# Performance work log

Measured on AMD Instinct MI355X. Metric: run time of the kernel, lower is better.

Reference implementation:

```python
import jax, jax.numpy as jnp
import numpy as np

N_HEAD = 16
NEG_BIG = 1e10  # matches the torch module's -10000000000.0 additive mask


def setup_inputs() -> dict:
    key = jax.random.key(0)
    k1, k2, k3 = jax.random.split(key, 3)
    B, T, D = 2, 2048, 1024
    x = jax.random.normal(k1, (B, T, D), dtype=jnp.float32)
    W_attn = jax.random.normal(k2, (D, 3 * D), dtype=jnp.float32) * 0.02
    b_attn = jnp.zeros((3 * D,), dtype=jnp.float32)
    W_proj = jax.random.normal(k3, (D, D), dtype=jnp.float32) * 0.02
    b_proj = jnp.zeros((D,), dtype=jnp.float32)
    return {"x": x, "W_attn": W_attn, "b_attn": b_attn,
            "W_proj": W_proj, "b_proj": b_proj}


def reference(x, W_attn, b_attn, W_proj, b_proj):
    B, T, D = x.shape
    H = N_HEAD
    dh = D // H
    # c_attn: fused qkv projection
    qkv = x @ W_attn + b_attn                      # [B, T, 3D]
    q, k, v = jnp.split(qkv, 3, axis=-1)
    # split heads -> [B, H, T, dh]
    q = q.reshape(B, T, H, dh).transpose(0, 2, 1, 3)
    k = k.reshape(B, T, H, dh).transpose(0, 2, 1, 3)
    v = v.reshape(B, T, H, dh).transpose(0, 2, 1, 3)
    # scores [B, H, T, T]
    w = jnp.einsum("bhqd,bhkd->bhqk", q, k)
    w = w / jnp.sqrt(jnp.float32(dh))              # scale=True
    # causal additive mask: w*b - 1e10*(1-b), b = lower-triangular ones
    bias = jnp.tril(jnp.ones((T, T), dtype=w.dtype))
    w = w * bias - NEG_BIG * (1.0 - bias)
    w = jax.nn.softmax(w, axis=-1)
    a = jnp.einsum("bhqk,bhkd->bhqd", w, v)        # [B, H, T, dh]
    # merge heads
    a = a.transpose(0, 2, 1, 3).reshape(B, T, D)
    # c_proj
    return a @ W_proj + b_proj
```

## Files before the change

### kernel.cpp

```cpp
#include <hip/hip_runtime.h>
#include <hip/hip_bf16.h>


typedef unsigned short u16;
typedef unsigned int u32;
typedef __attribute__((ext_vector_type(4))) float f32x4;
typedef __attribute__((ext_vector_type(16))) float f32x16;
typedef __attribute__((ext_vector_type(8))) short bf16x8;
typedef __attribute__((ext_vector_type(4))) int i32x4;

__device__ __forceinline__ u16 f2bf(float f) {
  unsigned u = __builtin_bit_cast(unsigned, f);
  u += 0x7FFFu + ((u >> 16) & 1u);
  return (u16)(u >> 16);
}

__device__ __forceinline__ u32 pack_bf2(float lo, float hi) {
  return (u32)f2bf(lo) | ((u32)f2bf(hi) << 16);
}

__device__ __forceinline__ void gl_lds16(const u16* g, u16* l) {
  __builtin_amdgcn_global_load_lds(
      (const __attribute__((address_space(1))) void*)g,
      (__attribute__((address_space(3))) void*)l, 16, 0, 0);
}

__global__ __launch_bounds__(256) void cast_bf16_kernel(const float* __restrict__ in,
                                                        u16* __restrict__ out, int n4) {
  int i = blockIdx.x * 256 + threadIdx.x;
  if (i < n4) {
    float4 f = reinterpret_cast<const float4*>(in)[i];
    ushort4 o;
    o.x = f2bf(f.x); o.y = f2bf(f.y); o.z = f2bf(f.z); o.w = f2bf(f.w);
    reinterpret_cast<ushort4*>(out)[i] = o;
  }
}

__global__ __launch_bounds__(256) void transpose_cast(const float* __restrict__ in,
                                                      u16* __restrict__ out, int R, int C) {
  __shared__ float tile[32][33];
  const int c0 = blockIdx.x * 32, r0 = blockIdx.y * 32;
  const int tx = threadIdx.x, ty = threadIdx.y;
#pragma unroll
  for (int i = 0; i < 4; ++i)
    tile[ty + 8 * i][tx] = in[(size_t)(r0 + ty + 8 * i) * C + c0 + tx];
  __syncthreads();
#pragma unroll
  for (int i = 0; i < 4; ++i)
    out[(size_t)(c0 + ty + 8 * i) * R + r0 + tx] = f2bf(tile[tx][ty + 8 * i]);
}

template <int MODE>
__global__ __launch_bounds__(256) void gemm_bf16(
    const u16* __restrict__ A, const u16* __restrict__ Bt, const float* __restrict__ bias,
    float* __restrict__ outF, u16* __restrict__ Qh, u16* __restrict__ Kh, u16* __restrict__ VhT,
    int M, int N, int K) {
  __shared__ u16 As[128 * 32];
  __shared__ u16 Bs[128 * 32];
  const int tid = threadIdx.x;
  const int wave = tid >> 6, lane = tid & 63;
  const int kg = lane >> 4, rr = lane & 15;
  const int wm = wave >> 1, wn = wave & 1;
  const int rowA0 = blockIdx.y * 128, colB0 = blockIdx.x * 128;

  const f32x4 z4 = {0.f, 0.f, 0.f, 0.f};
  f32x4 acc[4][4];
#pragma unroll
  for (int i = 0; i < 4; ++i)
#pragma unroll
    for (int j = 0; j < 4; ++j) acc[i][j] = z4;

  const int r_st = tid >> 2;
  const int c_st = (tid & 3) * 8;

  for (int k0 = 0; k0 < K; k0 += 32) {
#pragma unroll
    for (int i = 0; i < 2; ++i) {
      gl_lds16(A + (size_t)(rowA0 + i * 64 + r_st) * K + k0 + c_st,
               As + (i * 256 + (wave << 6)) * 8);
      gl_lds16(Bt + (size_t)(colB0 + i * 64 + r_st) * K + k0 + c_st,
               Bs + (i * 256 + (wave << 6)) * 8);
    }
    __syncthreads();

    bf16x8 af[4], bfr[4];
#pragma unroll
    for (int mi = 0; mi < 4; ++mi)
      af[mi] = *reinterpret_cast<const bf16x8*>(&As[(wm * 64 + mi * 16 + rr) * 32 + kg * 8]);
#pragma unroll
    for (int ni = 0; ni < 4; ++ni)
      bfr[ni] = *reinterpret_cast<const bf16x8*>(&Bs[(wn * 64 + ni * 16 + rr) * 32 + kg * 8]);
#pragma unroll
    for (int mi = 0; mi < 4; ++mi)
#pragma unroll
      for (int ni = 0; ni < 4; ++ni)
        acc[mi][ni] = __builtin_amdgcn_mfma_f32_16x16x32_bf16(af[mi], bfr[ni], acc[mi][ni], 0, 0, 0);
    __syncthreads();
  }

#pragma unroll
  for (int mi = 0; mi < 4; ++mi) {
#pragma unroll
    for (int ni = 0; ni < 4; ++ni) {
      const int col = colB0 + wn * 64 + ni * 16 + rr;
      const float bcol = bias[col];
      f32x4 a = acc[mi][ni];
#pragma unroll
      for (int v = 0; v < 4; ++v) {
        const int row = rowA0 + wm * 64 + mi * 16 + kg * 4 + v;
        const float val = a[v] + bcol;
        if (MODE == 1) {
          outF[(size_t)row * N + col] = val;
        } else {
          const int b = row >> 11, t = row & 2047;
          const int which = col >> 10, d = col & 1023;
          const int h = d >> 6, dd = d & 63;
          const size_t bh = (size_t)(b * 16 + h);
          if (which == 0)
            Qh[(bh * 2048 + t) * 64 + dd] = f2bf(val);
          else if (which == 1)
            Kh[(bh * 2048 + t) * 64 + dd] = f2bf(val);
          else
            VhT[(bh * 64 + dd) * 2048 + t] = f2bf(val);
        }
      }
    }
  }
}

__global__ __launch_bounds__(256) void attn_fwd(const u16* __restrict__ Qh,
                                                const u16* __restrict__ Kh,
                                                const u16* __restrict__ VhT,
                                                u16* __restrict__ Ab) {
  const int tid = threadIdx.x;
  const int wave = tid >> 6, lane = tid & 63;
  const int lq = lane & 31, hi = lane >> 5;
  const int task = blockIdx.x * 4 + wave;
  const int qi = task >> 5;
  const int bh = task & 31;
  const int qtile = 63 - qi;
  const int q0 = qtile * 32;
  const int myq = q0 + lq;
  const size_t kvbase = (size_t)bh * 2048;

  bf16x8 qf[4];
  {
    const u16* qptr = Qh + (kvbase + q0 + lq) * 64 + hi * 8;
#pragma unroll
    for (int ks = 0; ks < 4; ++ks)
      qf[ks] = *reinterpret_cast<const bf16x8*>(qptr + ks * 16);
  }

  f32x16 oA, oB;
#pragma unroll
  for (int i = 0; i < 16; ++i) { oA[i] = 0.f; oB[i] = 0.f; }
  float m = -1e30f, l = 0.f;

  const int n64 = (q0 + 32 + 63) >> 6;
  for (int kvb = 0; kvb < n64; ++kvb) {
    const int kv0 = kvb * 64;

    const u16* kptr = Kh + (kvbase + kv0 + lq) * 64 + hi * 8;
    bf16x8 kfA[4], kfB[4];
#pragma unroll
    for (int ks = 0; ks < 4; ++ks) {
      kfA[ks] = *reinterpret_cast<const bf16x8*>(kptr + ks * 16);
      kfB[ks] = *reinterpret_cast<const bf16x8*>(kptr + 2048 + ks * 16);
    }
    const u16* vptr = VhT + ((size_t)bh * 64 + lq) * 2048 + kv0 + hi * 8;
    bf16x8 vfA[4], vfB[4];
#pragma unroll
    for (int ks = 0; ks < 4; ++ks) {
      vfA[ks] = *reinterpret_cast<const bf16x8*>(vptr + ks * 16);
      vfB[ks] = *reinterpret_cast<const bf16x8*>(vptr + 32 * 2048 + ks * 16);
    }

    f32x16 sA, sB;
#pragma unroll
    for (int i = 0; i < 16; ++i) { sA[i] = 0.f; sB[i] = 0.f; }
#pragma unroll
    for (int ks = 0; ks < 4; ++ks)
      sA = __builtin_amdgcn_mfma_f32_32x32x16_bf16(kfA[ks], qf[ks], sA, 0, 0, 0);
#pragma unroll
    for (int ks = 0; ks < 4; ++ks)
      sB = __builtin_amdgcn_mfma_f32_32x32x16_bf16(kfB[ks], qf[ks], sB, 0, 0, 0);

    if (kvb == n64 - 1) {
#pragma unroll
      for (int r = 0; r < 16; ++r) {
        const int kvA = kv0 + (r & 3) + 8 * (r >> 2) + 4 * hi;
        if (kvA > myq) sA[r] = -1e30f;
        if (kvA + 32 > myq) sB[r] = -1e30f;
      }
    }

    float pmax = -1e30f;
#pragma unroll
    for (int r = 0; r < 16; ++r) pmax = fmaxf(pmax, fmaxf(sA[r], sB[r]));
    pmax = fmaxf(pmax, __shfl_xor(pmax, 32));
    const float mn = fmaxf(m, pmax);
    const float sc = __expf((m - mn) * 0.125f);
    const float mn8 = mn * 0.125f;
    float rsum = 0.f;
#pragma unroll
    for (int r = 0; r < 16; ++r) {
      const float pa = __expf(__builtin_fmaf(sA[r], 0.125f, -mn8));
      const float pb = __expf(__builtin_fmaf(sB[r], 0.125f, -mn8));
      sA[r] = pa; sB[r] = pb;
      rsum += pa + pb;
    }
    rsum += __shfl_xor(rsum, 32);
    l = l * sc + rsum;
    m = mn;
    oA *= sc;
    oB *= sc;

    u32 pkA[8], pkB[8];
#pragma unroll
    for (int i = 0; i < 8; ++i) {
      pkA[i] = pack_bf2(sA[2 * i], sA[2 * i + 1]);
      pkB[i] = pack_bf2(sB[2 * i], sB[2 * i + 1]);
    }
    bf16x8 pf[4];
    {
      auto w0 = __builtin_amdgcn_permlane32_swap(pkA[0], pkA[2], false, false);
      auto w1 = __builtin_amdgcn_permlane32_swap(pkA[1], pkA[3], false, false);
      i32x4 t0 = {(int)w0[0], (int)w1[0], (int)w0[1], (int)w1[1]};
      pf[0] = __builtin_bit_cast(bf16x8, t0);
      auto w2 = __builtin_amdgcn_permlane32_swap(pkA[4], pkA[6], false, false);
      auto w3 = __builtin_amdgcn_permlane32_swap(pkA[5], pkA[7], false, false);
      i32x4 t1 = {(int)w2[0], (int)w3[0], (int)w2[1], (int)w3[1]};
      pf[1] = __builtin_bit_cast(bf16x8, t1);
      auto w4 = __builtin_amdgcn_permlane32_swap(pkB[0], pkB[2], false, false);
      auto w5 = __builtin_amdgcn_permlane32_swap(pkB[1], pkB[3], false, false);
      i32x4 t2 = {(int)w4[0], (int)w5[0], (int)w4[1], (int)w5[1]};
      pf[2] = __builtin_bit_cast(bf16x8, t2);
      auto w6 = __builtin_amdgcn_permlane32_swap(pkB[4], pkB[6], false, false);
      auto w7 = __builtin_amdgcn_permlane32_swap(pkB[5], pkB[7], false, false);
      i32x4 t3 = {(int)w6[0], (int)w7[0], (int)w6[1], (int)w7[1]};
      pf[3] = __builtin_bit_cast(bf16x8, t3);
    }

#pragma unroll
    for (int ks = 0; ks < 4; ++ks)
      oA = __builtin_amdgcn_mfma_f32_32x32x16_bf16(vfA[ks], pf[ks], oA, 0, 0, 0);
#pragma unroll
    for (int ks = 0; ks < 4; ++ks)
      oB = __builtin_amdgcn_mfma_f32_32x32x16_bf16(vfB[ks], pf[ks], oB, 0, 0, 0);
  }

  const float inv = 1.0f / l;
  const int b = bh >> 4, h = bh & 15;
  u16* base = Ab + ((size_t)b * 2048 + myq) * 1024 + h * 64;
#pragma unroll
  for (int g = 0; g < 4; ++g) {
    const int dh0 = 8 * g + 4 * hi;
    ushort4 wa, wb;
    wa.x = f2bf(oA[4 * g + 0] * inv); wa.y = f2bf(oA[4 * g + 1] * inv);
    wa.z = f2bf(oA[4 * g + 2] * inv); wa.w = f2bf(oA[4 * g + 3] * inv);
    wb.x = f2bf(oB[4 * g + 0] * inv); wb.y = f2bf(oB[4 * g + 1] * inv);
    wb.z = f2bf(oB[4 * g + 2] * inv); wb.w = f2bf(oB[4 * g + 3] * inv);
    *reinterpret_cast<ushort4*>(base + dh0) = wa;
    *reinterpret_cast<ushort4*>(base + 32 + dh0) = wb;
  }
}

extern "C" void kernel_launch(void* const* d_in, const int* in_sizes, int n_in,
                              void* d_out, int out_size, void* d_ws, size_t ws_size,
                              hipStream_t stream) {
  const float* x      = (const float*)d_in[0];
  const float* W_attn = (const float*)d_in[1];
  const float* b_attn = (const float*)d_in[2];
  const float* W_proj = (const float*)d_in[3];
  const float* b_proj = (const float*)d_in[4];
  float* out = (float*)d_out;

  u16* xb  = (u16*)d_ws;
  u16* Wat = xb + (size_t)4096 * 1024;
  u16* Wpt = Wat + (size_t)3072 * 1024;
  u16* Qh  = Wpt + (size_t)1024 * 1024;
  u16* Kh  = Qh + (size_t)4194304;
  u16* VhT = Kh + (size_t)4194304;
  u16* Ab  = VhT + (size_t)4194304;

  cast_bf16_kernel<<<4096, 256, 0, stream>>>(x, xb, 4096 * 1024 / 4);
  transpose_cast<<<dim3(96, 32), dim3(32, 8), 0, stream>>>(W_attn, Wat, 1024, 3072);
  transpose_cast<<<dim3(32, 32), dim3(32, 8), 0, stream>>>(W_proj, Wpt, 1024, 1024);
  gemm_bf16<0><<<dim3(24, 32), 256, 0, stream>>>(xb, Wat, b_attn, nullptr, Qh, Kh, VhT,
                                                 4096, 3072, 1024);
  attn_fwd<<<dim3(512), 256, 0, stream>>>(Qh, Kh, VhT, Ab);
  gemm_bf16<1><<<dim3(8, 32), 256, 0, stream>>>(Ab, Wpt, b_proj, out, nullptr, nullptr, nullptr,
                                                4096, 1024, 1024);
}
```

Baseline: 247.1 us.

## Split attention KV range across waves, swizzle GEMM tiles, lazy softmax rescale

The attention kernel now gives each block one (q-tile, head) pair and splits its KV blocks across four waves. The per-wave partial max, sum and output are merged through LDS before a single store. This raises the block count from 512 to 2048 to improve load balance and occupancy for the causal triangle. The 1/8 softmax scale is folded into Q during the QKV GEMM, and the running-max rescale is skipped when the max grows by no more than 8, which is a lazy rescaling trick. Both GEMMs get an XCD-style block swizzle, and the projection GEMM uses narrower 128x64 tiles for more blocks. In exchange it adds LDS traffic, a sync, and a small bf16 accuracy change from prescaling Q.

Measured after the change: 225.5 us. 8.7% less time.

```diff
diff --git a/kernel.cpp b/kernel.cpp
--- a/kernel.cpp
+++ b/kernel.cpp
@@ -50,18 +50,20 @@
     out[(size_t)(c0 + ty + 8 * i) * R + r0 + tx] = f2bf(tile[tx][ty + 8 * i]);
 }
 
-template <int MODE>
-__global__ __launch_bounds__(256) void gemm_bf16(
+__global__ __launch_bounds__(256) void gemm_qkv(
     const u16* __restrict__ A, const u16* __restrict__ Bt, const float* __restrict__ bias,
-    float* __restrict__ outF, u16* __restrict__ Qh, u16* __restrict__ Kh, u16* __restrict__ VhT,
-    int M, int N, int K) {
+    u16* __restrict__ Qh, u16* __restrict__ Kh, u16* __restrict__ VhT, int K) {
   __shared__ u16 As[128 * 32];
   __shared__ u16 Bs[128 * 32];
   const int tid = threadIdx.x;
   const int wave = tid >> 6, lane = tid & 63;
   const int kg = lane >> 4, rr = lane & 15;
   const int wm = wave >> 1, wn = wave & 1;
-  const int rowA0 = blockIdx.y * 128, colB0 = blockIdx.x * 128;
+  const int nwg = gridDim.x * gridDim.y;
+  const int lin = blockIdx.y * gridDim.x + blockIdx.x;
+  const int swz = (lin & 7) * (nwg >> 3) + (lin >> 3);
+  const int bx = swz % gridDim.x, by = swz / gridDim.x;
+  const int rowA0 = by * 128, colB0 = bx * 128;
 
   const f32x4 z4 = {0.f, 0.f, 0.f, 0.f};
   f32x4 acc[4][4];
@@ -109,20 +111,79 @@
       for (int v = 0; v < 4; ++v) {
         const int row = rowA0 + wm * 64 + mi * 16 + kg * 4 + v;
         const float val = a[v] + bcol;
-        if (MODE == 1) {
-          outF[(size_t)row * N + col] = val;
-        } else {
-          const int b = row >> 11, t = row & 2047;
-          const int which = col >> 10, d = col & 1023;
-          const int h = d >> 6, dd = d & 63;
-          const size_t bh = (size_t)(b * 16 + h);
-          if (which == 0)
-            Qh[(bh * 2048 + t) * 64 + dd] = f2bf(val);
-          else if (which == 1)
-            Kh[(bh * 2048 + t) * 64 + dd] = f2bf(val);
-          else
-            VhT[(bh * 64 + dd) * 2048 + t] = f2bf(val);
-        }
+        const int b = row >> 11, t = row & 2047;
+        const int which = col >> 10, d = col & 1023;
+        const int h = d >> 6, dd = d & 63;
+        const size_t bh = (size_t)(b * 16 + h);
+        if (which == 0)
+          Qh[(bh * 2048 + t) * 64 + dd] = f2bf(val * 0.125f);
+        else if (which == 1)
+          Kh[(bh * 2048 + t) * 64 + dd] = f2bf(val);
+        else
+          VhT[(bh * 64 + dd) * 2048 + t] = f2bf(val);
+      }
+    }
+  }
+}
+
+__global__ __launch_bounds__(256) void gemm_proj(
+    const u16* __restrict__ A, const u16* __restrict__ Bt, const float* __restrict__ bias,
+    float* __restrict__ outF, int N, int K) {
+  __shared__ u16 As[128 * 32];
+  __shared__ u16 Bs[64 * 32];
+  const int tid = threadIdx.x;
+  const int wave = tid >> 6, lane = tid & 63;
+  const int kg = lane >> 4, rr = lane & 15;
+  const int nwg = gridDim.x * gridDim.y;
+  const int lin = blockIdx.y * gridDim.x + blockIdx.x;
+  const int swz = (lin & 7) * (nwg >> 3) + (lin >> 3);
+  const int bx = swz % gridDim.x, by = swz / gridDim.x;
+  const int rowA0 = by * 128, colB0 = bx * 64;
+
+  const f32x4 z4 = {0.f, 0.f, 0.f, 0.f};
+  f32x4 acc[2][4];
+#pragma unroll
+  for (int i = 0; i < 2; ++i)
+#pragma unroll
+    for (int j = 0; j < 4; ++j) acc[i][j] = z4;
+
+  const int r_st = tid >> 2;
+  const int c_st = (tid & 3) * 8;
+
+  for (int k0 = 0; k0 < K; k0 += 32) {
+#pragma unroll
+    for (int i = 0; i < 2; ++i)
+      gl_lds16(A + (size_t)(rowA0 + i * 64 + r_st) * K + k0 + c_st,
+               As + (i * 256 + (wave << 6)) * 8);
+    gl_lds16(Bt + (size_t)(colB0 + r_st) * K + k0 + c_st, Bs + (wave << 6) * 8);
+    __syncthreads();
+
+    bf16x8 af[2], bfr[4];
+#pragma unroll
+    for (int mi = 0; mi < 2; ++mi)
+      af[mi] = *reinterpret_cast<const bf16x8*>(&As[(wave * 32 + mi * 16 + rr) * 32 + kg * 8]);
+#pragma unroll
+    for (int ni = 0; ni < 4; ++ni)
+      bfr[ni] = *reinterpret_cast<const bf16x8*>(&Bs[(ni * 16 + rr) * 32 + kg * 8]);
+#pragma unroll
+    for (int mi = 0; mi < 2; ++mi)
+#pragma unroll
+      for (int ni = 0; ni < 4; ++ni)
+        acc[mi][ni] = __builtin_amdgcn_mfma_f32_16x16x32_bf16(af[mi], bfr[ni], acc[mi][ni], 0, 0, 0);
+    __syncthreads();
+  }
+
+#pragma unroll
+  for (int mi = 0; mi < 2; ++mi) {
+#pragma unroll
+    for (int ni = 0; ni < 4; ++ni) {
+      const int col = colB0 + ni * 16 + rr;
+      const float bcol = bias[col];
+      f32x4 a = acc[mi][ni];
+#pragma unroll
+      for (int v = 0; v < 4; ++v) {
+        const int row = rowA0 + wave * 32 + mi * 16 + kg * 4 + v;
+        outF[(size_t)row * N + col] = a[v] + bcol;
       }
     }
   }
@@ -132,17 +193,24 @@
                                                 const u16* __restrict__ Kh,
                                                 const u16* __restrict__ VhT,
                                                 u16* __restrict__ Ab) {
+  __shared__ float Ol[4][64][33];
+  __shared__ float Ml[4][2][32];
   const int tid = threadIdx.x;
   const int wave = tid >> 6, lane = tid & 63;
   const int lq = lane & 31, hi = lane >> 5;
-  const int task = blockIdx.x * 4 + wave;
-  const int qi = task >> 5;
-  const int bh = task & 31;
+  const int blk = blockIdx.x;
+  const int qi = blk >> 5;
+  const int bh = blk & 31;
   const int qtile = 63 - qi;
   const int q0 = qtile * 32;
   const int myq = q0 + lq;
   const size_t kvbase = (size_t)bh * 2048;
 
+  const int n64 = (q0 + 32 + 63) >> 6;
+  const int base = n64 >> 2, rem = n64 & 3;
+  const int cnt = base + (wave < rem ? 1 : 0);
+  const int start = wave * base + (wave < rem ? wave : rem);
+
   bf16x8 qf[4];
   {
     const u16* qptr = Qh + (kvbase + q0 + lq) * 64 + hi * 8;
@@ -156,8 +224,7 @@
   for (int i = 0; i < 16; ++i) { oA[i] = 0.f; oB[i] = 0.f; }
   float m = -1e30f, l = 0.f;
 
-  const int n64 = (q0 + 32 + 63) >> 6;
-  for (int kvb = 0; kvb < n64; ++kvb) {
+  for (int kvb = start; kvb < start + cnt; ++kvb) {
     const int kv0 = kvb * 64;
 
     const u16* kptr = Kh + (kvbase + kv0 + lq) * 64 + hi * 8;
@@ -198,22 +265,24 @@
 #pragma unroll
     for (int r = 0; r < 16; ++r) pmax = fmaxf(pmax, fmaxf(sA[r], sB[r]));
     pmax = fmaxf(pmax, __shfl_xor(pmax, 32));
-    const float mn = fmaxf(m, pmax);
-    const float sc = __expf((m - mn) * 0.125f);
-    const float mn8 = mn * 0.125f;
+    if (!__all(pmax - m <= 8.0f)) {
+      const float mn = fmaxf(m, pmax);
+      const float sc = __expf(m - mn);
+      l *= sc;
+      oA *= sc;
+      oB *= sc;
+      m = mn;
+    }
     float rsum = 0.f;
 #pragma unroll
     for (int r = 0; r < 16; ++r) {
-      const float pa = __expf(__builtin_fmaf(sA[r], 0.125f, -mn8));
-      const float pb = __expf(__builtin_fmaf(sB[r], 0.125f, -mn8));
+      const float pa = __expf(sA[r] - m);
+      const float pb = __expf(sB[r] - m);
       sA[r] = pa; sB[r] = pb;
       rsum += pa + pb;
     }
     rsum += __shfl_xor(rsum, 32);
-    l = l * sc + rsum;
-    m = mn;
-    oA *= sc;
-    oB *= sc;
+    l += rsum;
 
     u32 pkA[8], pkB[8];
 #pragma unroll
@@ -249,20 +318,48 @@
       oB = __builtin_amdgcn_mfma_f32_32x32x16_bf16(vfB[ks], pf[ks], oB, 0, 0, 0);
   }
 
-  const float inv = 1.0f / l;
+  if (hi == 0) {
+    Ml[wave][0][lq] = m;
+    Ml[wave][1][lq] = l;
+  }
+#pragma unroll
+  for (int r = 0; r < 16; ++r) {
+    const int dhA = (r & 3) + 8 * (r >> 2) + 4 * hi;
+    Ol[wave][dhA][lq] = oA[r];
+    Ol[wave][dhA + 32][lq] = oB[r];
+  }
+  __syncthreads();
+
+  const int col = tid >> 3;
+  const int dh0 = (tid & 7) * 8;
+  float mw[4];
+  float M = -1e30f;
+#pragma unroll
+  for (int w = 0; w < 4; ++w) { mw[w] = Ml[w][0][col]; M = fmaxf(M, mw[w]); }
+  float scw[4];
+  float lsum = 0.f;
+#pragma unroll
+  for (int w = 0; w < 4; ++w) {
+    scw[w] = __expf(mw[w] - M);
+    lsum += scw[w] * Ml[w][1][col];
+  }
+  const float inv = 1.0f / lsum;
   const int b = bh >> 4, h = bh & 15;
-  u16* base = Ab + ((size_t)b * 2048 + myq) * 1024 + h * 64;
-#pragma unroll
-  for (int g = 0; g < 4; ++g) {
-    const int dh0 = 8 * g + 4 * hi;
-    ushort4 wa, wb;
-    wa.x = f2bf(oA[4 * g + 0] * inv); wa.y = f2bf(oA[4 * g + 1] * inv);
-    wa.z = f2bf(oA[4 * g + 2] * inv); wa.w = f2bf(oA[4 * g + 3] * inv);
-    wb.x = f2bf(oB[4 * g + 0] * inv); wb.y = f2bf(oB[4 * g + 1] * inv);
-    wb.z = f2bf(oB[4 * g + 2] * inv); wb.w = f2bf(oB[4 * g + 3] * inv);
-    *reinterpret_cast<ushort4*>(base + dh0) = wa;
-    *reinterpret_cast<ushort4*>(base + 32 + dh0) = wb;
-  }
+  u16* dst = Ab + ((size_t)b * 2048 + q0 + col) * 1024 + h * 64 + dh0;
+  ushort4 w0, w1;
+  u16 tmp[8];
+#pragma unroll
+  for (int i = 0; i < 8; ++i) {
+    const int dh = dh0 + i;
+    float v = 0.f;
+#pragma unroll
+    for (int w = 0; w < 4; ++w) v += scw[w] * Ol[w][dh][col];
+    tmp[i] = f2bf(v * inv);
+  }
+  w0.x = tmp[0]; w0.y = tmp[1]; w0.z = tmp[2]; w0.w = tmp[3];
+  w1.x = tmp[4]; w1.y = tmp[5]; w1.z = tmp[6]; w1.w = tmp[7];
+  *reinterpret_cast<ushort4*>(dst) = w0;
+  *reinterpret_cast<ushort4*>(dst + 4) = w1;
 }
 
 extern "C" void kernel_launch(void* const* d_in, const int* in_sizes, int n_in,
@@ -286,9 +383,7 @@
   cast_bf16_kernel<<<4096, 256, 0, stream>>>(x, xb, 4096 * 1024 / 4);
   transpose_cast<<<dim3(96, 32), dim3(32, 8), 0, stream>>>(W_attn, Wat, 1024, 3072);
   transpose_cast<<<dim3(32, 32), dim3(32, 8), 0, stream>>>(W_proj, Wpt, 1024, 1024);
-  gemm_bf16<0><<<dim3(24, 32), 256, 0, stream>>>(xb, Wat, b_attn, nullptr, Qh, Kh, VhT,
-                                                 4096, 3072, 1024);
-  attn_fwd<<<dim3(512), 256, 0, stream>>>(Qh, Kh, VhT, Ab);
-  gemm_bf16<1><<<dim3(8, 32), 256, 0, stream>>>(Ab, Wpt, b_proj, out, nullptr, nullptr, nullptr,
-                                                4096, 1024, 1024);
-}
+  gemm_qkv<<<dim3(24, 32), 256, 0, stream>>>(xb, Wat, b_attn, Qh, Kh, VhT, 1024);
+  attn_fwd<<<dim3(2048), 256, 0, stream>>>(Qh, Kh, VhT, Ab);
+  gemm_proj<<<dim3(16, 32), 256, 0, stream>>>(Ab, Wpt, b_proj, out, 1024, 1024);
+}
```
